# Kernel tuning notes

Hardware: AMD Instinct MI355X
Metric: run time of the kernel (lower is better)

The kernel has to match this reference:

```python
import jax, jax.numpy as jnp
import numpy as np

N_NODES = 50000
N_EDGES = 400000
IN_DIM = 256
OUT_DIM = 64
HEADS = 2
ATTN_HIDDEN = 64
ALPHA = 0.2
TEMP = 0.55


def setup_inputs() -> dict:
    key = jax.random.key(0)
    k_x, k_src, k_dst, k_w, k_wa, k_a = jax.random.split(key, 6)
    x = jax.random.normal(k_x, (N_NODES, IN_DIM), dtype=jnp.float32)
    src = jax.random.randint(k_src, (N_EDGES,), 0, N_NODES, dtype=jnp.int32)
    dst = jnp.sort(jax.random.randint(k_dst, (N_EDGES,), 0, N_NODES, dtype=jnp.int32))
    # Glorot-uniform-like params
    def glorot(k, shape, fan_in, fan_out):
        lim = jnp.sqrt(6.0 / (fan_in + fan_out))
        return jax.random.uniform(k, shape, jnp.float32, -lim, lim)
    W = glorot(k_w, (IN_DIM, HEADS, OUT_DIM), IN_DIM, HEADS * OUT_DIM)
    W_attn = glorot(k_wa, (HEADS, 2 * OUT_DIM, ATTN_HIDDEN), 2 * OUT_DIM, ATTN_HIDDEN)
    a_vec = glorot(k_a, (HEADS, ATTN_HIDDEN), HEADS, ATTN_HIDDEN)
    return {"x": x, "W": W, "W_attn": W_attn, "a_vec": a_vec, "src": src, "dst": dst}


def reference(x, W, W_attn, a_vec, src, dst):
    N = x.shape[0]
    # node-level projection: [N, H, F]
    Wh = jnp.einsum('nd,dhf->nhf', x, W)
    # per-edge gathers
    Wh_src = Wh[src]                                   # [E, H, F]
    Wh_dst = Wh[dst]                                   # [E, H, F]
    z = jnp.concatenate([Wh_src, Wh_dst], axis=-1)     # [E, H, 2F]
    z_act = jax.nn.leaky_relu(jnp.einsum('ehf,hfc->ehc', z, W_attn), ALPHA)
    logits = jnp.einsum('ehc,hc->eh', z_act, a_vec).astype(jnp.float32) / TEMP
    # per-head segment softmax over incoming edges of each dst node
    seg_max = jax.ops.segment_max(logits, dst, num_segments=N)   # [N, H]
    ex = jnp.exp(logits - seg_max[dst])
    seg_sum = jax.ops.segment_sum(ex, dst, num_segments=N)
    alphas = (ex / (seg_sum[dst] + 1e-9)).astype(Wh_src.dtype)   # [E, H]
    # weighted scatter-sum of source messages
    out = jax.ops.segment_sum(Wh_src * alphas[..., None], dst, num_segments=N)  # [N, H, F]
    # concat=False -> mean over heads (dropout is identity at inference)
    return out.mean(axis=1)
```

## Files before the change

### kernel.cpp

```cpp
#include <hip/hip_runtime.h>
#include <hip/hip_bf16.h>
#include <math.h>

#define N_NODES 50000
#define N_EDGES 400000
#define IN_DIM 256
#define OUT_DIM 64
#define HEADS 2
#define ATTN_HIDDEN 64
#define ALPHA_SLOPE 0.2f
#define TEMP 0.55f
#define NHF 128
#define ZDIM 384

typedef __bf16 bf16x8 __attribute__((ext_vector_type(8)));
typedef float f32x4 __attribute__((ext_vector_type(4)));

__device__ __forceinline__ ushort f2bf(float f) {
    unsigned u = __float_as_uint(f);
    u = (u + 0x7fffu + ((u >> 16) & 1u)) >> 16;
    return (ushort)u;
}
__device__ __forceinline__ unsigned pack2(float a, float b) {
    return (unsigned)f2bf(a) | ((unsigned)f2bf(b) << 16);
}
__device__ __forceinline__ float bfl(unsigned u) { return __uint_as_float(u << 16); }
__device__ __forceinline__ float bfh(unsigned u) { return __uint_as_float(u & 0xffff0000u); }

__global__ __launch_bounds__(256) void k_combine(const float* __restrict__ W,
                                                 const float* __restrict__ Wa,
                                                 ushort* __restrict__ Wctf,
                                                 const int* __restrict__ dst,
                                                 int* __restrict__ seg) {
    __shared__ float col[64];
    const int b = blockIdx.x;
    const int t = threadIdx.x;
    if (b >= ZDIM) {
        int n = (b - ZDIM) * 256 + t;
        if (n > N_NODES) return;
        int lo = 0, hi = N_EDGES;
        while (lo < hi) {
            int mid = (lo + hi) >> 1;
            if (dst[mid] < n) lo = mid + 1; else hi = mid;
        }
        seg[n] = lo;
        return;
    }
    const int n = b;
    const int k = t;
    const int c = n >> 4, r16 = n & 15;
    const int kc = k >> 5, q = (k >> 3) & 3, j = k & 7;
    const size_t pos = (size_t)(((c * 8 + kc) * 64 + q * 16 + r16)) * 8 + j;

    float val;
    if (n < 128) {
        val = W[(size_t)k * NHF + n];
    } else {
        const int part = (n - 128) >> 7;
        const int idx = (n - 128) & 127;
        const int h = idx >> 6;
        const int cc = idx & 63;
        const int fb = part ? 64 : 0;
        if (t < 64) col[t] = Wa[(size_t)h * 8192 + (size_t)(fb + t) * 64 + cc];
        __syncthreads();
        const float* wr = W + (size_t)k * NHF + h * 64;
        float acc = 0.f;
#pragma unroll
        for (int f = 0; f < 64; f++) acc += wr[f] * col[f];
        val = acc;
    }
    Wctf[pos] = f2bf(val);
}

__global__ __launch_bounds__(256, 2) void k_gemm(const float* __restrict__ x,
                                                 const ushort* __restrict__ Wctf,
                                                 ushort* __restrict__ Zb) {
    __shared__ __align__(16) ushort Bs[32768];
    const int t = threadIdx.x;
    const int w = t >> 6, lane = t & 63;
    const int q = lane >> 4, r16 = lane & 15;
    const int rowbase = blockIdx.x * 64 + w * 16;

    {
        const uint4* gs = (const uint4*)Wctf;
        uint4* ls = (uint4*)Bs;
#pragma unroll
        for (int i = 0; i < 16; i++) ls[i * 256 + t] = gs[i * 256 + t];
    }

    int rA = rowbase + r16;
    rA = rA < N_NODES ? rA : N_NODES - 1;
    const float* xp = x + (size_t)rA * IN_DIM + q * 8;
    uint4 Areg[8];
#pragma unroll
    for (int kc = 0; kc < 8; kc++) {
        const float4 a0 = *(const float4*)(xp + kc * 32);
        const float4 a1 = *(const float4*)(xp + kc * 32 + 4);
        Areg[kc].x = pack2(a0.x, a0.y); Areg[kc].y = pack2(a0.z, a0.w);
        Areg[kc].z = pack2(a1.x, a1.y); Areg[kc].w = pack2(a1.z, a1.w);
    }

    __syncthreads();

#pragma unroll 1
    for (int s = 0; s < 3; s++) {
        f32x4 acc[8];
#pragma unroll
        for (int c = 0; c < 8; c++) acc[c] = (f32x4){0.f, 0.f, 0.f, 0.f};

#pragma unroll
        for (int kc = 0; kc < 8; kc++) {
            const bf16x8 af = *(const bf16x8*)&Areg[kc];
#pragma unroll
            for (int c = 0; c < 8; c++) {
                const bf16x8 bf = *(const bf16x8*)&Bs[((c * 8 + kc) * 64 + lane) * 8];
                acc[c] = __builtin_amdgcn_mfma_f32_16x16x32_bf16(af, bf, acc[c], 0, 0, 0);
            }
        }

        if (s < 2) {
            __syncthreads();
            const uint4* gs = (const uint4*)Wctf + (size_t)(s + 1) * 4096;
            uint4* ls = (uint4*)Bs;
#pragma unroll
            for (int i = 0; i < 16; i++) ls[i * 256 + t] = gs[i * 256 + t];
        }

#pragma unroll
        for (int c = 0; c < 8; c++)
#pragma unroll
            for (int rr = 0; rr < 4; rr++) {
                const int row = rowbase + q * 4 + rr;
                if (row < N_NODES)
                    Zb[(size_t)row * ZDIM + (s * 8 + c) * 16 + r16] = f2bf(acc[c][rr]);
            }

        if (s < 2) __syncthreads();
    }
}

__global__ __launch_bounds__(256) void k_fused(const ushort* __restrict__ Zb,
                                               const float* __restrict__ avec,
                                               const int* __restrict__ src,
                                               const int* __restrict__ seg,
                                               float* __restrict__ out) {
    const int lane = threadIdx.x & 63;
    const int wv = threadIdx.x >> 6;
    const int g = lane >> 4, l16 = lane & 15;
    const int n = blockIdx.x * 16 + wv * 4 + g;
    if (n >= N_NODES) return;
    const int choff = 8 * l16;

    const float4 af0 = *(const float4*)(avec + choff);
    const float4 af1 = *(const float4*)(avec + choff + 4);
    const float a[8] = {af0.x, af0.y, af0.z, af0.w, af1.x, af1.y, af1.z, af1.w};

    const uint4 udv = *(const uint4*)(Zb + (size_t)n * ZDIM + 256 + choff);
    const float ud[8] = {bfl(udv.x), bfh(udv.x), bfl(udv.y), bfh(udv.y),
                         bfl(udv.z), bfh(udv.z), bfl(udv.w), bfh(udv.w)};

    const int e0 = seg[n], e1 = seg[n + 1];
    float m = -INFINITY, l = 0.f;
    float acc[8] = {0.f, 0.f, 0.f, 0.f, 0.f, 0.f, 0.f, 0.f};

    uint4 us = make_uint4(0, 0, 0, 0), wh = us;
    if (e0 < e1) {
        const int s = src[e0];
        us = *(const uint4*)(Zb + (size_t)s * ZDIM + 128 + choff);
        wh = *(const uint4*)(Zb + (size_t)s * ZDIM + choff);
    }
    for (int e = e0; e < e1; e++) {
        const uint4 cus = us, cwh = wh;
        if (e + 1 < e1) {
            const int sn = src[e + 1];
            us = *(const uint4*)(Zb + (size_t)sn * ZDIM + 128 + choff);
            wh = *(const uint4*)(Zb + (size_t)sn * ZDIM + choff);
        }
        float p;
        {
            float v0, v1, s0, s1;
            v0 = bfl(cus.x) + ud[0]; v1 = bfh(cus.x) + ud[1];
            s0 = fmaxf(v0, ALPHA_SLOPE * v0); s1 = fmaxf(v1, ALPHA_SLOPE * v1);
            p = s0 * a[0] + s1 * a[1];
            v0 = bfl(cus.y) + ud[2]; v1 = bfh(cus.y) + ud[3];
            s0 = fmaxf(v0, ALPHA_SLOPE * v0); s1 = fmaxf(v1, ALPHA_SLOPE * v1);
            p += s0 * a[2] + s1 * a[3];
            v0 = bfl(cus.z) + ud[4]; v1 = bfh(cus.z) + ud[5];
            s0 = fmaxf(v0, ALPHA_SLOPE * v0); s1 = fmaxf(v1, ALPHA_SLOPE * v1);
            p += s0 * a[4] + s1 * a[5];
            v0 = bfl(cus.w) + ud[6]; v1 = bfh(cus.w) + ud[7];
            s0 = fmaxf(v0, ALPHA_SLOPE * v0); s1 = fmaxf(v1, ALPHA_SLOPE * v1);
            p += s0 * a[6] + s1 * a[7];
        }
        p += __shfl_xor(p, 1, 64);
        p += __shfl_xor(p, 2, 64);
        p += __shfl_xor(p, 4, 64);
        const float logit = p * (1.0f / TEMP);
        const float nm = fmaxf(m, logit);
        const float sc = __expf(m - nm);
        const float wgt = __expf(logit - nm);
        l = l * sc + wgt;
        acc[0] = acc[0] * sc + wgt * bfl(cwh.x);
        acc[1] = acc[1] * sc + wgt * bfh(cwh.x);
        acc[2] = acc[2] * sc + wgt * bfl(cwh.y);
        acc[3] = acc[3] * sc + wgt * bfh(cwh.y);
        acc[4] = acc[4] * sc + wgt * bfl(cwh.z);
        acc[5] = acc[5] * sc + wgt * bfh(cwh.z);
        acc[6] = acc[6] * sc + wgt * bfl(cwh.w);
        acc[7] = acc[7] * sc + wgt * bfh(cwh.w);
        m = nm;
    }
    const float inv = 0.5f / (l + 1e-9f);
#pragma unroll
    for (int j = 0; j < 8; j++) {
        const float v = acc[j] * inv;
        acc[j] = v + __shfl_xor(v, 8, 64);
    }
    if (l16 < 8) {
        float4 o0 = make_float4(acc[0], acc[1], acc[2], acc[3]);
        float4 o1 = make_float4(acc[4], acc[5], acc[6], acc[7]);
        float* op = out + (size_t)n * 64 + choff;
        *(float4*)op = o0;
        *(float4*)(op + 4) = o1;
    }
}

extern "C" void kernel_launch(void* const* d_in, const int* in_sizes, int n_in,
                              void* d_out, int out_size, void* d_ws, size_t ws_size,
                              hipStream_t stream) {
    const float* x    = (const float*)d_in[0];
    const float* W    = (const float*)d_in[1];
    const float* Wa   = (const float*)d_in[2];
    const float* avec = (const float*)d_in[3];
    const int*   src  = (const int*)d_in[4];
    const int*   dst  = (const int*)d_in[5];
    float* out = (float*)d_out;

    ushort* Zb   = (ushort*)d_ws;
    ushort* Wctf = Zb + 19200000;
    int*    seg  = (int*)((char*)d_ws + 38596608);

    const int seg_blocks = (N_NODES + 1 + 255) / 256;
    k_combine <<<ZDIM + seg_blocks, 256, 0, stream>>>(W, Wa, Wctf, dst, seg);
    k_gemm    <<<(N_NODES + 63) / 64, 256, 0, stream>>>(x, Wctf, Zb);
    k_fused   <<<(N_NODES + 15) / 16, 256, 0, stream>>>(Zb, avec, src, seg, out);
}
```

Before: 157.2 us.

## Halve GEMM LDS tile for occupancy and give each edge-lane sixteen channels

The projection GEMM now stages a 32 KB B tile in six passes instead of a 64 KB tile in three, and raises launch bounds to 4 blocks per CU so more waves can hide the x loads. The fused edge kernel maps 8 lanes per node, each handling 16 channels, so 8 nodes share a wave instead of 4. This halves the shuffle-reduction depth and doubles the independent node streams per wave to better hide gather latency. The GEMM adds extra barriers and B reloads, and the edge kernel uses more registers per lane.

```diff
diff --git a/kernel.cpp b/kernel.cpp
--- a/kernel.cpp
+++ b/kernel.cpp
@@ -72,10 +72,10 @@
     Wctf[pos] = f2bf(val);
 }
 
-__global__ __launch_bounds__(256, 2) void k_gemm(const float* __restrict__ x,
+__global__ __launch_bounds__(256, 4) void k_gemm(const float* __restrict__ x,
                                                  const ushort* __restrict__ Wctf,
                                                  ushort* __restrict__ Zb) {
-    __shared__ __align__(16) ushort Bs[32768];
+    __shared__ __align__(16) ushort Bs[16384];
     const int t = threadIdx.x;
     const int w = t >> 6, lane = t & 63;
     const int q = lane >> 4, r16 = lane & 15;
@@ -85,7 +85,7 @@
         const uint4* gs = (const uint4*)Wctf;
         uint4* ls = (uint4*)Bs;
 #pragma unroll
-        for (int i = 0; i < 16; i++) ls[i * 256 + t] = gs[i * 256 + t];
+        for (int i = 0; i < 8; i++) ls[i * 256 + t] = gs[i * 256 + t];
     }
 
     int rA = rowbase + r16;
@@ -103,39 +103,39 @@
     __syncthreads();
 
 #pragma unroll 1
-    for (int s = 0; s < 3; s++) {
-        f32x4 acc[8];
-#pragma unroll
-        for (int c = 0; c < 8; c++) acc[c] = (f32x4){0.f, 0.f, 0.f, 0.f};
+    for (int s = 0; s < 6; s++) {
+        f32x4 acc[4];
+#pragma unroll
+        for (int c = 0; c < 4; c++) acc[c] = (f32x4){0.f, 0.f, 0.f, 0.f};
 
 #pragma unroll
         for (int kc = 0; kc < 8; kc++) {
             const bf16x8 af = *(const bf16x8*)&Areg[kc];
 #pragma unroll
-            for (int c = 0; c < 8; c++) {
+            for (int c = 0; c < 4; c++) {
                 const bf16x8 bf = *(const bf16x8*)&Bs[((c * 8 + kc) * 64 + lane) * 8];
                 acc[c] = __builtin_amdgcn_mfma_f32_16x16x32_bf16(af, bf, acc[c], 0, 0, 0);
             }
         }
 
-        if (s < 2) {
+        if (s < 5) {
             __syncthreads();
-            const uint4* gs = (const uint4*)Wctf + (size_t)(s + 1) * 4096;
+            const uint4* gs = (const uint4*)Wctf + (size_t)(s + 1) * 2048;
             uint4* ls = (uint4*)Bs;
 #pragma unroll
-            for (int i = 0; i < 16; i++) ls[i * 256 + t] = gs[i * 256 + t];
-        }
-
-#pragma unroll
-        for (int c = 0; c < 8; c++)
+            for (int i = 0; i < 8; i++) ls[i * 256 + t] = gs[i * 256 + t];
+        }
+
+#pragma unroll
+        for (int c = 0; c < 4; c++)
 #pragma unroll
             for (int rr = 0; rr < 4; rr++) {
                 const int row = rowbase + q * 4 + rr;
                 if (row < N_NODES)
-                    Zb[(size_t)row * ZDIM + (s * 8 + c) * 16 + r16] = f2bf(acc[c][rr]);
+                    Zb[(size_t)row * ZDIM + (s * 4 + c) * 16 + r16] = f2bf(acc[c][rr]);
             }
 
-        if (s < 2) __syncthreads();
+        if (s < 5) __syncthreads();
     }
 }
 
@@ -146,82 +146,89 @@
                                                float* __restrict__ out) {
     const int lane = threadIdx.x & 63;
     const int wv = threadIdx.x >> 6;
-    const int g = lane >> 4, l16 = lane & 15;
-    const int n = blockIdx.x * 16 + wv * 4 + g;
+    const int g = lane >> 3, l8 = lane & 7;
+    const int n = blockIdx.x * 32 + wv * 8 + g;
     if (n >= N_NODES) return;
-    const int choff = 8 * l16;
-
-    const float4 af0 = *(const float4*)(avec + choff);
-    const float4 af1 = *(const float4*)(avec + choff + 4);
-    const float a[8] = {af0.x, af0.y, af0.z, af0.w, af1.x, af1.y, af1.z, af1.w};
-
-    const uint4 udv = *(const uint4*)(Zb + (size_t)n * ZDIM + 256 + choff);
-    const float ud[8] = {bfl(udv.x), bfh(udv.x), bfl(udv.y), bfh(udv.y),
-                         bfl(udv.z), bfh(udv.z), bfl(udv.w), bfh(udv.w)};
+    const int choff = 16 * l8;
+
+    float a[16], ud[16];
+#pragma unroll
+    for (int i = 0; i < 4; i++) {
+        const float4 av = *(const float4*)(avec + choff + 4 * i);
+        a[4 * i] = av.x; a[4 * i + 1] = av.y; a[4 * i + 2] = av.z; a[4 * i + 3] = av.w;
+    }
+    {
+        const uint4 u0 = *(const uint4*)(Zb + (size_t)n * ZDIM + 256 + choff);
+        const uint4 u1 = *(const uint4*)(Zb + (size_t)n * ZDIM + 256 + choff + 8);
+        ud[0] = bfl(u0.x); ud[1] = bfh(u0.x); ud[2] = bfl(u0.y); ud[3] = bfh(u0.y);
+        ud[4] = bfl(u0.z); ud[5] = bfh(u0.z); ud[6] = bfl(u0.w); ud[7] = bfh(u0.w);
+        ud[8] = bfl(u1.x); ud[9] = bfh(u1.x); ud[10] = bfl(u1.y); ud[11] = bfh(u1.y);
+        ud[12] = bfl(u1.z); ud[13] = bfh(u1.z); ud[14] = bfl(u1.w); ud[15] = bfh(u1.w);
+    }
 
     const int e0 = seg[n], e1 = seg[n + 1];
     float m = -INFINITY, l = 0.f;
-    float acc[8] = {0.f, 0.f, 0.f, 0.f, 0.f, 0.f, 0.f, 0.f};
-
-    uint4 us = make_uint4(0, 0, 0, 0), wh = us;
+    float acc[16];
+#pragma unroll
+    for (int j = 0; j < 16; j++) acc[j] = 0.f;
+
+    uint4 us0 = make_uint4(0,0,0,0), us1 = us0, wh0 = us0, wh1 = us0;
     if (e0 < e1) {
         const int s = src[e0];
-        us = *(const uint4*)(Zb + (size_t)s * ZDIM + 128 + choff);
-        wh = *(const uint4*)(Zb + (size_t)s * ZDIM + choff);
+        us0 = *(const uint4*)(Zb + (size_t)s * ZDIM + 128 + choff);
+        us1 = *(const uint4*)(Zb + (size_t)s * ZDIM + 128 + choff + 8);
+        wh0 = *(const uint4*)(Zb + (size_t)s * ZDIM + choff);
+        wh1 = *(const uint4*)(Zb + (size_t)s * ZDIM + choff + 8);
     }
     for (int e = e0; e < e1; e++) {
-        const uint4 cus = us, cwh = wh;
+        const uint4 cu0 = us0, cu1 = us1, cw0 = wh0, cw1 = wh1;
         if (e + 1 < e1) {
             const int sn = src[e + 1];
-            us = *(const uint4*)(Zb + (size_t)sn * ZDIM + 128 + choff);
-            wh = *(const uint4*)(Zb + (size_t)sn * ZDIM + choff);
-        }
-        float p;
-        {
-            float v0, v1, s0, s1;
-            v0 = bfl(cus.x) + ud[0]; v1 = bfh(cus.x) + ud[1];
-            s0 = fmaxf(v0, ALPHA_SLOPE * v0); s1 = fmaxf(v1, ALPHA_SLOPE * v1);
-            p = s0 * a[0] + s1 * a[1];
-            v0 = bfl(cus.y) + ud[2]; v1 = bfh(cus.y) + ud[3];
-            s0 = fmaxf(v0, ALPHA_SLOPE * v0); s1 = fmaxf(v1, ALPHA_SLOPE * v1);
-            p += s0 * a[2] + s1 * a[3];
-            v0 = bfl(cus.z) + ud[4]; v1 = bfh(cus.z) + ud[5];
-            s0 = fmaxf(v0, ALPHA_SLOPE * v0); s1 = fmaxf(v1, ALPHA_SLOPE * v1);
-            p += s0 * a[4] + s1 * a[5];
-            v0 = bfl(cus.w) + ud[6]; v1 = bfh(cus.w) + ud[7];
-            s0 = fmaxf(v0, ALPHA_SLOPE * v0); s1 = fmaxf(v1, ALPHA_SLOPE * v1);
-            p += s0 * a[6] + s1 * a[7];
+            us0 = *(const uint4*)(Zb + (size_t)sn * ZDIM + 128 + choff);
+            us1 = *(const uint4*)(Zb + (size_t)sn * ZDIM + 128 + choff + 8);
+            wh0 = *(const uint4*)(Zb + (size_t)sn * ZDIM + choff);
+            wh1 = *(const uint4*)(Zb + (size_t)sn * ZDIM + choff + 8);
+        }
+        float us[16];
+        us[0] = bfl(cu0.x); us[1] = bfh(cu0.x); us[2] = bfl(cu0.y); us[3] = bfh(cu0.y);
+        us[4] = bfl(cu0.z); us[5] = bfh(cu0.z); us[6] = bfl(cu0.w); us[7] = bfh(cu0.w);
+        us[8] = bfl(cu1.x); us[9] = bfh(cu1.x); us[10] = bfl(cu1.y); us[11] = bfh(cu1.y);
+        us[12] = bfl(cu1.z); us[13] = bfh(cu1.z); us[14] = bfl(cu1.w); us[15] = bfh(cu1.w);
+        float p = 0.f;
+#pragma unroll
+        for (int j = 0; j < 16; j++) {
+            const float v = us[j] + ud[j];
+            p += fmaxf(v, ALPHA_SLOPE * v) * a[j];
         }
         p += __shfl_xor(p, 1, 64);
         p += __shfl_xor(p, 2, 64);
-        p += __shfl_xor(p, 4, 64);
         const float logit = p * (1.0f / TEMP);
         const float nm = fmaxf(m, logit);
         const float sc = __expf(m - nm);
         const float wgt = __expf(logit - nm);
         l = l * sc + wgt;
-        acc[0] = acc[0] * sc + wgt * bfl(cwh.x);
-        acc[1] = acc[1] * sc + wgt * bfh(cwh.x);
-        acc[2] = acc[2] * sc + wgt * bfl(cwh.y);
-        acc[3] = acc[3] * sc + wgt * bfh(cwh.y);
-        acc[4] = acc[4] * sc + wgt * bfl(cwh.z);
-        acc[5] = acc[5] * sc + wgt * bfh(cwh.z);
-        acc[6] = acc[6] * sc + wgt * bfl(cwh.w);
-        acc[7] = acc[7] * sc + wgt * bfh(cwh.w);
+        float wh[16];
+        wh[0] = bfl(cw0.x); wh[1] = bfh(cw0.x); wh[2] = bfl(cw0.y); wh[3] = bfh(cw0.y);
+        wh[4] = bfl(cw0.z); wh[5] = bfh(cw0.z); wh[6] = bfl(cw0.w); wh[7] = bfh(cw0.w);
+        wh[8] = bfl(cw1.x); wh[9] = bfh(cw1.x); wh[10] = bfl(cw1.y); wh[11] = bfh(cw1.y);
+        wh[12] = bfl(cw1.z); wh[13] = bfh(cw1.z); wh[14] = bfl(cw1.w); wh[15] = bfh(cw1.w);
+#pragma unroll
+        for (int j = 0; j < 16; j++) acc[j] = acc[j] * sc + wgt * wh[j];
         m = nm;
     }
     const float inv = 0.5f / (l + 1e-9f);
 #pragma unroll
-    for (int j = 0; j < 8; j++) {
+    for (int j = 0; j < 16; j++) {
         const float v = acc[j] * inv;
-        acc[j] = v + __shfl_xor(v, 8, 64);
-    }
-    if (l16 < 8) {
-        float4 o0 = make_float4(acc[0], acc[1], acc[2], acc[3]);
-        float4 o1 = make_float4(acc[4], acc[5], acc[6], acc[7]);
+        acc[j] = v + __shfl_xor(v, 4, 64);
+    }
+    if (l8 < 4) {
         float* op = out + (size_t)n * 64 + choff;
-        *(float4*)op = o0;
-        *(float4*)(op + 4) = o1;
+#pragma unroll
+        for (int i = 0; i < 4; i++) {
+            float4 o = make_float4(acc[4 * i], acc[4 * i + 1], acc[4 * i + 2], acc[4 * i + 3]);
+            *(float4*)(op + 4 * i) = o;
+        }
     }
 }
 
@@ -243,5 +250,5 @@
     const int seg_blocks = (N_NODES + 1 + 255) / 256;
     k_combine <<<ZDIM + seg_blocks, 256, 0, stream>>>(W, Wa, Wctf, dst, seg);
     k_gemm    <<<(N_NODES + 63) / 64, 256, 0, stream>>>(x, Wctf, Zb);
-    k_fused   <<<(N_NODES + 15) / 16, 256, 0, stream>>>(Zb, avec, src, seg, out);
-}
+    k_fused   <<<(N_NODES + 31) / 32, 256, 0, stream>>>(Zb, avec, src, seg, out);
+}
```

Result: slower. 161.2 us (+2.6%).
